# Optimization experiments

Measured on AMD Instinct MI355X. Metric: run time of the kernel, lower is better.

Reference implementation:

```python
import jax, jax.numpy as jnp
import numpy as np

EMBED_DIM = 1024
NB_HEADS = 16
HEAD_DIM = EMBED_DIM // NB_HEADS


def setup_inputs() -> dict:
    key = jax.random.key(0)
    ks = jax.random.split(key, 5)
    B, N, D = 4, 2048, EMBED_DIM
    scale = 1.0 / np.sqrt(D)
    return {
        "x": jax.random.normal(ks[0], (B, N, D), dtype=jnp.float32),
        "qkv_w": jax.random.normal(ks[1], (3 * D, D), dtype=jnp.float32) * scale,
        "qkv_b": jax.random.normal(ks[2], (3 * D,), dtype=jnp.float32) * 0.02,
        "proj_w": jax.random.normal(ks[3], (D, D), dtype=jnp.float32) * scale,
        "proj_b": jax.random.normal(ks[4], (D,), dtype=jnp.float32) * 0.02,
    }


def reference(x, qkv_w, qkv_b, proj_w, proj_b):
    B, N, D = x.shape
    H, Hd = NB_HEADS, HEAD_DIM
    # qkv projection: torch Linear => x @ W.T + b
    qkv = x @ qkv_w.T + qkv_b                       # [B, N, 3D]
    qkv = qkv.reshape(B, N, 3, H, Hd)
    q = jnp.transpose(qkv[:, :, 0], (0, 2, 1, 3))   # [B, H, N, Hd]
    k = jnp.transpose(qkv[:, :, 1], (0, 2, 1, 3))
    v = jnp.transpose(qkv[:, :, 2], (0, 2, 1, 3))
    scores = jnp.einsum("bhnd,bhmd->bhnm", q, k) * (Hd ** -0.5)  # [B,H,N,N]
    attn = jax.nn.softmax(scores, axis=-1)
    out = jnp.einsum("bhnm,bhmd->bhnd", attn, v)    # [B, H, N, Hd]
    out = jnp.transpose(out, (0, 2, 1, 3)).reshape(B, N, D)
    out = out @ proj_w.T + proj_b
    return out
```

## Files before the change

### kernel.cpp

```cpp
#include <hip/hip_runtime.h>


typedef __attribute__((ext_vector_type(8))) short bf16x8;
typedef __attribute__((ext_vector_type(4))) short s16x4;
typedef __attribute__((ext_vector_type(4))) float f32x4;
typedef __attribute__((ext_vector_type(16))) float f32x16;
typedef __attribute__((ext_vector_type(4))) unsigned u32x4;

#define LOG2E 1.44269504088896340736f

__device__ static inline short f2bf(float f) {
  unsigned u = __builtin_bit_cast(unsigned, f);
  unsigned r = (u + 0x7fffu + ((u >> 16) & 1u)) >> 16;
  return (short)r;
}
__device__ static inline unsigned cvtpk_bf16(float lo, float hi) {
  unsigned r;
  asm("v_cvt_pk_bf16_f32 %0, %1, %2" : "=v"(r) : "v"(lo), "v"(hi));
  return r;
}

__device__ static inline void gload_lds16(const void* g, void* l) {
  __builtin_amdgcn_global_load_lds(
      (const __attribute__((address_space(1))) void*)g,
      (__attribute__((address_space(3))) void*)l, 16, 0, 0);
}

__global__ void cvt_f32_bf16(const float* __restrict__ in, short* __restrict__ out, int n4) {
  int i = blockIdx.x * 256 + threadIdx.x;
  if (i < n4) {
    float4 v = ((const float4*)in)[i];
    s16x4 o4 = { f2bf(v.x), f2bf(v.y), f2bf(v.z), f2bf(v.w) };
    ((s16x4*)out)[i] = o4;
  }
}

template <int EPI>
__global__ __launch_bounds__(256, 2) void gemm_bt(
    const short* __restrict__ A, const short* __restrict__ Bm,
    const float* __restrict__ bias, int K,
    short* __restrict__ qo, short* __restrict__ ko, short* __restrict__ vto,
    float* __restrict__ outf) {
  __shared__ __align__(16) char smem[16384];
  char* As = smem;
  char* Bs = smem + 8192;
  const int tid = threadIdx.x, lane = tid & 63, w = tid >> 6;
  const int wm = w >> 1, wn = w & 1;
  const int bm = blockIdx.y, bn = blockIdx.x;

  f32x4 acc[4][4];
  const f32x4 z4 = {0.f, 0.f, 0.f, 0.f};
#pragma unroll
  for (int m = 0; m < 4; ++m)
#pragma unroll
    for (int n = 0; n < 4; ++n) acc[m][n] = z4;

  const short* Abase = A + (size_t)bm * 128 * K;
  const short* Bbase = Bm + (size_t)bn * 128 * K;

  for (int k0 = 0; k0 < K; k0 += 32) {
#pragma unroll
    for (int j = 0; j < 2; ++j) {
      int ia = w * 2 + j;
      int row = ia * 16 + (lane >> 2);
      int cl = (lane & 3) ^ (row & 3);
      gload_lds16(Abase + (size_t)row * K + k0 + cl * 8, As + ia * 1024);
      gload_lds16(Bbase + (size_t)row * K + k0 + cl * 8, Bs + ia * 1024);
    }
    __syncthreads();

    bf16x8 af[4], bf[4];
#pragma unroll
    for (int m = 0; m < 4; ++m) {
      int r = wm * 64 + m * 16 + (lane & 15);
      af[m] = *(const bf16x8*)(As + r * 64 + ((((lane >> 4)) ^ (r & 3)) << 4));
    }
#pragma unroll
    for (int n = 0; n < 4; ++n) {
      int r = wn * 64 + n * 16 + (lane & 15);
      bf[n] = *(const bf16x8*)(Bs + r * 64 + ((((lane >> 4)) ^ (r & 3)) << 4));
    }
#pragma unroll
    for (int m = 0; m < 4; ++m)
#pragma unroll
      for (int n = 0; n < 4; ++n)
        acc[m][n] = __builtin_amdgcn_mfma_f32_16x16x32_bf16(af[m], bf[n], acc[m][n], 0, 0, 0);
    __syncthreads();
  }

  if (EPI == 0) {
    const int which = bn >> 3;
    const int hh = ((bn & 7) << 1) | wn;
    const int bidx = bm >> 4;
    const size_t bh = (size_t)bidx * 16 + hh;
#pragma unroll
    for (int nf = 0; nf < 4; ++nf) {
      int dd = nf * 16 + (lane & 15);
      float bv = bias[bn * 128 + wn * 64 + dd];
#pragma unroll
      for (int m = 0; m < 4; ++m) {
        int nr0 = (bm & 15) * 128 + wm * 64 + m * 16 + ((lane >> 4) << 2);
        if (which == 2) {
          int nper = (nr0 & ~12) | ((nr0 & 4) << 1) | ((nr0 & 8) >> 1);
          s16x4 pk;
#pragma unroll
          for (int r = 0; r < 4; ++r) pk[r] = f2bf(acc[m][nf][r] + bv);
          *(s16x4*)(vto + (bh * 64 + dd) * 2048 + nper) = pk;
        } else if (which == 0) {
          short* dst = qo + (bh * 2048 + nr0) * 64 + dd;
#pragma unroll
          for (int r = 0; r < 4; ++r)
            dst[(size_t)r * 64] = f2bf((acc[m][nf][r] + bv) * (0.125f * LOG2E));
        } else {
          short* dst = ko + (bh * 2048 + nr0) * 64 + dd;
#pragma unroll
          for (int r = 0; r < 4; ++r) dst[(size_t)r * 64] = f2bf(acc[m][nf][r] + bv);
        }
      }
    }
  } else {
#pragma unroll
    for (int nf = 0; nf < 4; ++nf) {
      int gn = bn * 128 + wn * 64 + nf * 16 + (lane & 15);
      float bv = bias[gn];
#pragma unroll
      for (int m = 0; m < 4; ++m) {
        int gm0 = bm * 128 + wm * 64 + m * 16 + ((lane >> 4) << 2);
        float* dst = outf + (size_t)gm0 * 1024 + gn;
#pragma unroll
        for (int r = 0; r < 4; ++r) dst[(size_t)r * 1024] = acc[m][nf][r] + bv;
      }
    }
  }
}

#define BUILD_PF(pf, sX0, sX1)                                                 \
  {                                                                            \
    u32x4 wd0 = {cvtpk_bf16(sX0[0], sX0[1]), cvtpk_bf16(sX0[2], sX0[3]),       \
                 cvtpk_bf16(sX0[4], sX0[5]), cvtpk_bf16(sX0[6], sX0[7])};      \
    pf[0] = __builtin_bit_cast(bf16x8, wd0);                                   \
    u32x4 wd1 = {cvtpk_bf16(sX0[8], sX0[9]), cvtpk_bf16(sX0[10], sX0[11]),     \
                 cvtpk_bf16(sX0[12], sX0[13]), cvtpk_bf16(sX0[14], sX0[15])};  \
    pf[1] = __builtin_bit_cast(bf16x8, wd1);                                   \
    u32x4 wd2 = {cvtpk_bf16(sX1[0], sX1[1]), cvtpk_bf16(sX1[2], sX1[3]),       \
                 cvtpk_bf16(sX1[4], sX1[5]), cvtpk_bf16(sX1[6], sX1[7])};      \
    pf[2] = __builtin_bit_cast(bf16x8, wd2);                                   \
    u32x4 wd3 = {cvtpk_bf16(sX1[8], sX1[9]), cvtpk_bf16(sX1[10], sX1[11]),     \
                 cvtpk_bf16(sX1[12], sX1[13]), cvtpk_bf16(sX1[14], sX1[15])};  \
    pf[3] = __builtin_bit_cast(bf16x8, wd3);                                   \
  }

__global__ __launch_bounds__(256, 2) void attn_kernel(
    const short* __restrict__ q, const short* __restrict__ kk,
    const short* __restrict__ vt, short* __restrict__ ao) {
  __shared__ __align__(16) char smem[32768];
  const int tid = threadIdx.x, lane = tid & 63, w = tid >> 6;
  const int r31 = lane & 31, h = lane >> 5;
  const int id = blockIdx.x;
  const int xcd = id & 7, p = id >> 3;
  const int bh = xcd * 8 + (p >> 3);
  const int qblk = p & 7;
  const int q0 = qblk * 256 + w * 64;

  const short* qptr = q + ((size_t)bh * 2048 + q0 + r31) * 64 + h * 8;
  const short* kgl = kk + (size_t)bh * 2048 * 64;
  const short* vgl = vt + (size_t)bh * 64 * 2048;

  const int srow = w * 16 + (lane >> 3);
  const int scol = ((lane & 7) * 8) ^ ((lane >> 3) << 3);
  const int ldst = w * 2048;

  bf16x8 qfA[4], qfB[4];
#pragma unroll
  for (int dk = 0; dk < 4; ++dk) {
    qfA[dk] = *(const bf16x8*)(qptr + dk * 16);
    qfB[dk] = *(const bf16x8*)(qptr + 32 * 64 + dk * 16);
  }

  f32x16 oA0, oA1, oB0, oB1;
#pragma unroll
  for (int e = 0; e < 16; ++e) { oA0[e] = 0.f; oA1[e] = 0.f; oB0[e] = 0.f; oB1[e] = 0.f; }
  float lsA[8], lsB[8];
#pragma unroll
  for (int e = 0; e < 8; ++e) { lsA[e] = 0.f; lsB[e] = 0.f; }

#pragma unroll
  for (int j = 0; j < 2; ++j) {
    gload_lds16(kgl + (size_t)(srow + j * 8) * 64 + scol, smem + ldst + j * 1024);
    gload_lds16(vgl + (size_t)(srow + j * 8) * 2048 + scol, smem + 8192 + ldst + j * 1024);
  }
  __syncthreads();

  int cur = 0;
  for (int t = 0; t < 2048; t += 64) {
    const char* Kb = smem + cur * 16384;
    const char* Vb = smem + cur * 16384 + 8192;

    if (t + 64 < 2048) {
      char* nb = (char*)smem + (cur ^ 1) * 16384;
#pragma unroll
      for (int j = 0; j < 2; ++j) {
        gload_lds16(kgl + (size_t)(t + 64 + srow + j * 8) * 64 + scol, nb + ldst + j * 1024);
        gload_lds16(vgl + (size_t)(srow + j * 8) * 2048 + (t + 64) + scol, nb + 8192 + ldst + j * 1024);
      }
    }

    bf16x8 kf0[4], kf1[4];
#pragma unroll
    for (int dk = 0; dk < 4; ++dk) {
      int cb = (dk * 32 + h * 16) ^ ((r31 & 7) << 4);
      kf0[dk] = *(const bf16x8*)(Kb + r31 * 128 + cb);
      kf1[dk] = *(const bf16x8*)(Kb + (32 + r31) * 128 + cb);
    }

    f32x16 sA0, sA1, sB0, sB1;
#pragma unroll
    for (int e = 0; e < 16; ++e) { sA0[e] = 0.f; sA1[e] = 0.f; sB0[e] = 0.f; sB1[e] = 0.f; }
#pragma unroll
    for (int dk = 0; dk < 4; ++dk) {
      sA0 = __builtin_amdgcn_mfma_f32_32x32x16_bf16(kf0[dk], qfA[dk], sA0, 0, 0, 0);
      sA1 = __builtin_amdgcn_mfma_f32_32x32x16_bf16(kf1[dk], qfA[dk], sA1, 0, 0, 0);
      sB0 = __builtin_amdgcn_mfma_f32_32x32x16_bf16(kf0[dk], qfB[dk], sB0, 0, 0, 0);
      sB1 = __builtin_amdgcn_mfma_f32_32x32x16_bf16(kf1[dk], qfB[dk], sB1, 0, 0, 0);
    }

    bf16x8 vf[8];
#pragma unroll
    for (int db = 0; db < 2; ++db)
#pragma unroll
      for (int ks = 0; ks < 4; ++ks) {
        int cb = (ks * 32 + h * 16) ^ ((r31 & 7) << 4);
        vf[db * 4 + ks] = *(const bf16x8*)(Vb + (db * 32 + r31) * 128 + cb);
      }

#pragma unroll
    for (int e = 0; e < 16; ++e) {
      sA0[e] = __builtin_exp2f(sA0[e]);
      sA1[e] = __builtin_exp2f(sA1[e]);
      sB0[e] = __builtin_exp2f(sB0[e]);
      sB1[e] = __builtin_exp2f(sB1[e]);
    }
#pragma unroll
    for (int e = 0; e < 8; ++e) {
      lsA[e] += (sA0[e] + sA0[e + 8]) + (sA1[e] + sA1[e + 8]);
      lsB[e] += (sB0[e] + sB0[e + 8]) + (sB1[e] + sB1[e + 8]);
    }

    bf16x8 pfA[4], pfB[4];
    BUILD_PF(pfA, sA0, sA1);
    BUILD_PF(pfB, sB0, sB1);

#pragma unroll
    for (int ks = 0; ks < 4; ++ks) {
      oA0 = __builtin_amdgcn_mfma_f32_32x32x16_bf16(vf[ks], pfA[ks], oA0, 0, 0, 0);
      oA1 = __builtin_amdgcn_mfma_f32_32x32x16_bf16(vf[4 + ks], pfA[ks], oA1, 0, 0, 0);
      oB0 = __builtin_amdgcn_mfma_f32_32x32x16_bf16(vf[ks], pfB[ks], oB0, 0, 0, 0);
      oB1 = __builtin_amdgcn_mfma_f32_32x32x16_bf16(vf[4 + ks], pfB[ks], oB1, 0, 0, 0);
    }

    __syncthreads();
    cur ^= 1;
  }

  const int b = bh >> 4, hd = bh & 15;
#pragma unroll
  for (int st = 4; st >= 1; st >>= 1)
#pragma unroll
    for (int e = 0; e < 4; ++e)
      if (e < st) { lsA[e] += lsA[e + st]; lsB[e] += lsB[e + st]; }
  float lsumA = lsA[0] + __shfl_xor(lsA[0], 32);
  float lsumB = lsB[0] + __shfl_xor(lsB[0], 32);
  float invA = 1.f / lsumA, invB = 1.f / lsumB;

  short* orowA = ao + ((size_t)b * 2048 + q0 + r31) * 1024 + hd * 64;
  short* orowB = orowA + (size_t)32 * 1024;
#pragma unroll
  for (int s2 = 0; s2 < 4; ++s2) {
    s16x4 a0, a1, b0, b1;
#pragma unroll
    for (int r = 0; r < 4; ++r) {
      a0[r] = f2bf(oA0[4 * s2 + r] * invA);
      a1[r] = f2bf(oA1[4 * s2 + r] * invA);
      b0[r] = f2bf(oB0[4 * s2 + r] * invB);
      b1[r] = f2bf(oB1[4 * s2 + r] * invB);
    }
    *(s16x4*)(orowA + 8 * s2 + 4 * h) = a0;
    *(s16x4*)(orowA + 32 + 8 * s2 + 4 * h) = a1;
    *(s16x4*)(orowB + 8 * s2 + 4 * h) = b0;
    *(s16x4*)(orowB + 32 + 8 * s2 + 4 * h) = b1;
  }
}

extern "C" void kernel_launch(void* const* d_in, const int* in_sizes, int n_in,
                              void* d_out, int out_size, void* d_ws, size_t ws_size,
                              hipStream_t stream) {
  const float* x = (const float*)d_in[0];
  const float* qkv_w = (const float*)d_in[1];
  const float* qkv_b = (const float*)d_in[2];
  const float* proj_w = (const float*)d_in[3];
  const float* proj_b = (const float*)d_in[4];
  float* out = (float*)d_out;

  char* ws = (char*)d_ws;
  short* xb    = (short*)(ws + 0);
  short* wqkv  = (short*)(ws + 16777216);
  short* wproj = (short*)(ws + 23068672);
  short* qb    = (short*)(ws + 25165824);
  short* kb    = (short*)(ws + 41943040);
  short* vtb   = (short*)(ws + 58720256);
  short* aob   = (short*)(ws + 75497472);

  cvt_f32_bf16<<<8192, 256, 0, stream>>>(x, xb, 2097152);
  cvt_f32_bf16<<<3072, 256, 0, stream>>>(qkv_w, wqkv, 786432);
  cvt_f32_bf16<<<1024, 256, 0, stream>>>(proj_w, wproj, 262144);

  gemm_bt<0><<<dim3(24, 64), 256, 0, stream>>>(xb, wqkv, qkv_b, 1024, qb, kb, vtb, nullptr);
  attn_kernel<<<512, 256, 0, stream>>>(qb, kb, vtb, aob);
  gemm_bt<1><<<dim3(8, 64), 256, 0, stream>>>(aob, wproj, proj_b, 1024, nullptr, nullptr, nullptr, out);
}
```

Baseline: 211.0 us.

## Split attention tile into two halves to interleave exp with MFMA, add setprio

Splits the per-iteration score computation into two 32-key halves, so the exp2/bf16 packing of one half can overlap the MFMAs of the other. Raises wave priority around the MFMA blocks with s_setprio and unrolls the KV loop by two. The aim is to hide VALU softmax work behind matrix-core work. Register pressure may rise from the unroll, and reordering only pays off if the compiler and hardware actually interleave the two halves.

New measurement: 213.7 us. About the same (+1.3%).

```diff
diff --git a/kernel.cpp b/kernel.cpp
--- a/kernel.cpp
+++ b/kernel.cpp
@@ -134,20 +134,14 @@
   }
 }
 
-#define BUILD_PF(pf, sX0, sX1)                                                 \
+#define BUILD_PF2(d0, d1, sv)                                                  \
   {                                                                            \
-    u32x4 wd0 = {cvtpk_bf16(sX0[0], sX0[1]), cvtpk_bf16(sX0[2], sX0[3]),       \
-                 cvtpk_bf16(sX0[4], sX0[5]), cvtpk_bf16(sX0[6], sX0[7])};      \
-    pf[0] = __builtin_bit_cast(bf16x8, wd0);                                   \
-    u32x4 wd1 = {cvtpk_bf16(sX0[8], sX0[9]), cvtpk_bf16(sX0[10], sX0[11]),     \
-                 cvtpk_bf16(sX0[12], sX0[13]), cvtpk_bf16(sX0[14], sX0[15])};  \
-    pf[1] = __builtin_bit_cast(bf16x8, wd1);                                   \
-    u32x4 wd2 = {cvtpk_bf16(sX1[0], sX1[1]), cvtpk_bf16(sX1[2], sX1[3]),       \
-                 cvtpk_bf16(sX1[4], sX1[5]), cvtpk_bf16(sX1[6], sX1[7])};      \
-    pf[2] = __builtin_bit_cast(bf16x8, wd2);                                   \
-    u32x4 wd3 = {cvtpk_bf16(sX1[8], sX1[9]), cvtpk_bf16(sX1[10], sX1[11]),     \
-                 cvtpk_bf16(sX1[12], sX1[13]), cvtpk_bf16(sX1[14], sX1[15])};  \
-    pf[3] = __builtin_bit_cast(bf16x8, wd3);                                   \
+    u32x4 w0_ = {cvtpk_bf16(sv[0], sv[1]), cvtpk_bf16(sv[2], sv[3]),           \
+                 cvtpk_bf16(sv[4], sv[5]), cvtpk_bf16(sv[6], sv[7])};          \
+    d0 = __builtin_bit_cast(bf16x8, w0_);                                      \
+    u32x4 w1_ = {cvtpk_bf16(sv[8], sv[9]), cvtpk_bf16(sv[10], sv[11]),         \
+                 cvtpk_bf16(sv[12], sv[13]), cvtpk_bf16(sv[14], sv[15])};      \
+    d1 = __builtin_bit_cast(bf16x8, w1_);                                      \
   }
 
 __global__ __launch_bounds__(256, 2) void attn_kernel(
@@ -192,6 +186,7 @@
   __syncthreads();
 
   int cur = 0;
+#pragma unroll 2
   for (int t = 0; t < 2048; t += 64) {
     const char* Kb = smem + cur * 16384;
     const char* Vb = smem + cur * 16384 + 8192;
@@ -213,16 +208,27 @@
       kf1[dk] = *(const bf16x8*)(Kb + (32 + r31) * 128 + cb);
     }
 
-    f32x16 sA0, sA1, sB0, sB1;
-#pragma unroll
-    for (int e = 0; e < 16; ++e) { sA0[e] = 0.f; sA1[e] = 0.f; sB0[e] = 0.f; sB1[e] = 0.f; }
+    f32x16 sA0, sB0;
+#pragma unroll
+    for (int e = 0; e < 16; ++e) { sA0[e] = 0.f; sB0[e] = 0.f; }
+    __builtin_amdgcn_s_setprio(1);
 #pragma unroll
     for (int dk = 0; dk < 4; ++dk) {
       sA0 = __builtin_amdgcn_mfma_f32_32x32x16_bf16(kf0[dk], qfA[dk], sA0, 0, 0, 0);
+      sB0 = __builtin_amdgcn_mfma_f32_32x32x16_bf16(kf0[dk], qfB[dk], sB0, 0, 0, 0);
+    }
+    __builtin_amdgcn_s_setprio(0);
+
+    f32x16 sA1, sB1;
+#pragma unroll
+    for (int e = 0; e < 16; ++e) { sA1[e] = 0.f; sB1[e] = 0.f; }
+    __builtin_amdgcn_s_setprio(1);
+#pragma unroll
+    for (int dk = 0; dk < 4; ++dk) {
       sA1 = __builtin_amdgcn_mfma_f32_32x32x16_bf16(kf1[dk], qfA[dk], sA1, 0, 0, 0);
-      sB0 = __builtin_amdgcn_mfma_f32_32x32x16_bf16(kf0[dk], qfB[dk], sB0, 0, 0, 0);
       sB1 = __builtin_amdgcn_mfma_f32_32x32x16_bf16(kf1[dk], qfB[dk], sB1, 0, 0, 0);
     }
+    __builtin_amdgcn_s_setprio(0);
 
     bf16x8 vf[8];
 #pragma unroll
@@ -236,27 +242,52 @@
 #pragma unroll
     for (int e = 0; e < 16; ++e) {
       sA0[e] = __builtin_exp2f(sA0[e]);
+      sB0[e] = __builtin_exp2f(sB0[e]);
+    }
+#pragma unroll
+    for (int e = 0; e < 8; ++e) {
+      lsA[e] += sA0[e] + sA0[e + 8];
+      lsB[e] += sB0[e] + sB0[e + 8];
+    }
+    bf16x8 pfA0, pfA1, pfB0, pfB1;
+    BUILD_PF2(pfA0, pfA1, sA0);
+    BUILD_PF2(pfB0, pfB1, sB0);
+
+    __builtin_amdgcn_s_setprio(1);
+    oA0 = __builtin_amdgcn_mfma_f32_32x32x16_bf16(vf[0], pfA0, oA0, 0, 0, 0);
+    oA1 = __builtin_amdgcn_mfma_f32_32x32x16_bf16(vf[4], pfA0, oA1, 0, 0, 0);
+    oB0 = __builtin_amdgcn_mfma_f32_32x32x16_bf16(vf[0], pfB0, oB0, 0, 0, 0);
+    oB1 = __builtin_amdgcn_mfma_f32_32x32x16_bf16(vf[4], pfB0, oB1, 0, 0, 0);
+    oA0 = __builtin_amdgcn_mfma_f32_32x32x16_bf16(vf[1], pfA1, oA0, 0, 0, 0);
+    oA1 = __builtin_amdgcn_mfma_f32_32x32x16_bf16(vf[5], pfA1, oA1, 0, 0, 0);
+    oB0 = __builtin_amdgcn_mfma_f32_32x32x16_bf16(vf[1], pfB1, oB0, 0, 0, 0);
+    oB1 = __builtin_amdgcn_mfma_f32_32x32x16_bf16(vf[5], pfB1, oB1, 0, 0, 0);
+    __builtin_amdgcn_s_setprio(0);
+
+#pragma unroll
+    for (int e = 0; e < 16; ++e) {
       sA1[e] = __builtin_exp2f(sA1[e]);
-      sB0[e] = __builtin_exp2f(sB0[e]);
       sB1[e] = __builtin_exp2f(sB1[e]);
     }
 #pragma unroll
     for (int e = 0; e < 8; ++e) {
-      lsA[e] += (sA0[e] + sA0[e + 8]) + (sA1[e] + sA1[e + 8]);
-      lsB[e] += (sB0[e] + sB0[e + 8]) + (sB1[e] + sB1[e + 8]);
-    }
-
-    bf16x8 pfA[4], pfB[4];
-    BUILD_PF(pfA, sA0, sA1);
-    BUILD_PF(pfB, sB0, sB1);
-
-#pragma unroll
-    for (int ks = 0; ks < 4; ++ks) {
-      oA0 = __builtin_amdgcn_mfma_f32_32x32x16_bf16(vf[ks], pfA[ks], oA0, 0, 0, 0);
-      oA1 = __builtin_amdgcn_mfma_f32_32x32x16_bf16(vf[4 + ks], pfA[ks], oA1, 0, 0, 0);
-      oB0 = __builtin_amdgcn_mfma_f32_32x32x16_bf16(vf[ks], pfB[ks], oB0, 0, 0, 0);
-      oB1 = __builtin_amdgcn_mfma_f32_32x32x16_bf16(vf[4 + ks], pfB[ks], oB1, 0, 0, 0);
-    }
+      lsA[e] += sA1[e] + sA1[e + 8];
+      lsB[e] += sB1[e] + sB1[e + 8];
+    }
+    bf16x8 pfA2, pfA3, pfB2, pfB3;
+    BUILD_PF2(pfA2, pfA3, sA1);
+    BUILD_PF2(pfB2, pfB3, sB1);
+
+    __builtin_amdgcn_s_setprio(1);
+    oA0 = __builtin_amdgcn_mfma_f32_32x32x16_bf16(vf[2], pfA2, oA0, 0, 0, 0);
+    oA1 = __builtin_amdgcn_mfma_f32_32x32x16_bf16(vf[6], pfA2, oA1, 0, 0, 0);
+    oB0 = __builtin_amdgcn_mfma_f32_32x32x16_bf16(vf[2], pfB2, oB0, 0, 0, 0);
+    oB1 = __builtin_amdgcn_mfma_f32_32x32x16_bf16(vf[6], pfB2, oB1, 0, 0, 0);
+    oA0 = __builtin_amdgcn_mfma_f32_32x32x16_bf16(vf[3], pfA3, oA0, 0, 0, 0);
+    oA1 = __builtin_amdgcn_mfma_f32_32x32x16_bf16(vf[7], pfA3, oA1, 0, 0, 0);
+    oB0 = __builtin_amdgcn_mfma_f32_32x32x16_bf16(vf[3], pfB3, oB0, 0, 0, 0);
+    oB1 = __builtin_amdgcn_mfma_f32_32x32x16_bf16(vf[7], pfB3, oB1, 0, 0, 0);
+    __builtin_amdgcn_s_setprio(0);
 
     __syncthreads();
     cur ^= 1;
```
